# Optimization experiments

Hardware: AMD Instinct MI355X
Metric: run time of the kernel (lower is better)

The kernel has to match this reference:

```python
import jax, jax.numpy as jnp
import numpy as np


def _lin(x, w, b):
    return x @ w + b


def _fmv(x, w):
    # fused weighted mean/variance over the views axis (dim 2)
    mean = jnp.sum(x * w, axis=2, keepdims=True)
    var = jnp.sum(w * (x - mean) ** 2, axis=2, keepdims=True)
    return mean, var


def setup_inputs() -> dict:
    key = jax.random.key(0)
    ks = iter(jax.random.split(key, 40))
    R, S, V = 2048, 64, 8  # n_rays, n_samples, n_views

    def W(i, o):
        return jax.random.normal(next(ks), (i, o), jnp.float32) * (1.0 / np.sqrt(i))

    inp = {
        "rgb_feat": jax.random.normal(next(ks), (R, S, V, 35), jnp.float32),
        "neuray_feat": jax.random.normal(next(ks), (R, S, V, 32), jnp.float32),
        "ray_diff": jax.random.normal(next(ks), (R, S, V, 4), jnp.float32),
        "mask": (jax.random.uniform(next(ks), (R, S, V, 1)) > 0.1).astype(jnp.float32),
        "que_pts": jax.random.normal(next(ks), (R, S, 3), jnp.float32),
        "que_dir": jax.random.normal(next(ks), (R, S, 3), jnp.float32),
        # ray_dir_fc: Linear(4,16) ELU Linear(16,35) ELU
        "rd_w1": W(4, 16), "rd_b1": jnp.zeros(16, jnp.float32),
        "rd_w2": W(16, 35), "rd_b2": jnp.zeros(35, jnp.float32),
        # rgbfeat_fc: Linear(35,64) ReLU Linear(64,64)
        "rf_w1": W(35, 64), "rf_b1": jnp.zeros(64, jnp.float32),
        "rf_w2": W(64, 64), "rf_b2": jnp.zeros(64, jnp.float32),
        # neuray_fc: Linear(32,8) ELU Linear(8,1)
        "nr_w1": W(32, 8), "nr_b1": jnp.zeros(8, jnp.float32),
        "nr_w2": W(8, 1), "nr_b2": jnp.zeros(1, jnp.float32),
        # base_fc: Linear(207,64) ELU Linear(64,32) ELU
        "base_w1": W(207, 64), "base_b1": jnp.zeros(64, jnp.float32),
        "base_w2": W(64, 32), "base_b2": jnp.zeros(32, jnp.float32),
        # vis_fc: Linear(32,32) ELU Linear(32,33) ELU
        "vis_w1": W(32, 32), "vis_b1": jnp.zeros(32, jnp.float32),
        "vis_w2": W(32, 33), "vis_b2": jnp.zeros(33, jnp.float32),
        # vis_fc2: Linear(32,32) ELU Linear(32,1) Sigmoid
        "v2_w1": W(32, 32), "v2_b1": jnp.zeros(32, jnp.float32),
        "v2_w2": W(32, 1), "v2_b2": jnp.zeros(1, jnp.float32),
    }
    return inp


def reference(rgb_feat, neuray_feat, ray_diff, mask, que_pts, que_dir,
              rd_w1, rd_b1, rd_w2, rd_b2,
              rf_w1, rf_b1, rf_w2, rf_b2,
              nr_w1, nr_b1, nr_w2, nr_b2,
              base_w1, base_b1, base_w2, base_b2,
              vis_w1, vis_b1, vis_w2, vis_b2,
              v2_w1, v2_b1, v2_w2, v2_b2):
    elu = jax.nn.elu
    num_views = rgb_feat.shape[2]

    direction_feat = elu(_lin(elu(_lin(ray_diff, rd_w1, rd_b1)), rd_w2, rd_b2))
    rgb_feat_ = rgb_feat + direction_feat  # [R,S,V,35]

    rgb_feat_1 = _lin(jax.nn.relu(_lin(rgb_feat, rf_w1, rf_b1)), rf_w2, rf_b2)
    rgb_feat_max = jnp.max(rgb_feat_1, axis=2)  # [R,S,64]

    weight = mask / (jnp.sum(mask, axis=2, keepdims=True) + 1e-8)
    weight0 = jax.nn.sigmoid(_lin(elu(_lin(neuray_feat, nr_w1, nr_b1)), nr_w2, nr_b2))

    mean0, var0 = _fmv(rgb_feat_, weight0)
    mean1, var1 = _fmv(rgb_feat_, weight)
    globalfeat = jnp.concatenate([mean0, var0, mean1, var1], axis=-1)  # [R,S,1,140]

    gshape = globalfeat.shape[:2] + (num_views, globalfeat.shape[-1])
    x = jnp.concatenate([jnp.broadcast_to(globalfeat, gshape), rgb_feat_, neuray_feat], axis=-1)  # [R,S,V,207]
    x = elu(_lin(elu(_lin(x, base_w1, base_b1)), base_w2, base_b2))  # [R,S,V,32]

    x_vis = elu(_lin(elu(_lin(x * weight, vis_w1, vis_b1)), vis_w2, vis_b2))  # [R,S,V,33]
    x_res, vis = x_vis[..., :-1], x_vis[..., -1:]
    vis = jax.nn.sigmoid(vis) * mask
    x = x + x_res
    vis = jax.nn.sigmoid(_lin(elu(_lin(x * vis, v2_w1, v2_b1)), v2_w2, v2_b2)) * mask
    weight2 = vis / (jnp.sum(vis, axis=2, keepdims=True) + 1e-8)

    mean, var = _fmv(x, weight2)
    out = jnp.concatenate([mean[:, :, 0], var[:, :, 0]], axis=-1) + rgb_feat_max  # [R,S,64]
    return out
```

## Files before the change

### kernel.cpp

```cpp
#include <hip/hip_runtime.h>


#define NRS (2048*64)

__device__ __forceinline__ float eluf(float x){ return x > 0.f ? x : __expf(x)-1.f; }
__device__ __forceinline__ float sigmf(float x){ return 1.f/(1.f+__expf(-x)); }
__device__ __forceinline__ float sum8(float x){
    x += __shfl_xor(x, 1); x += __shfl_xor(x, 2); x += __shfl_xor(x, 4); return x;
}
__device__ __forceinline__ float max8(float x){
    x = fmaxf(x, __shfl_xor(x, 1)); x = fmaxf(x, __shfl_xor(x, 2)); x = fmaxf(x, __shfl_xor(x, 4)); return x;
}

__global__ __launch_bounds__(64, 2) void nerf_main(
    const float* __restrict__ g_rgb,  const float* __restrict__ g_nr,
    const float* __restrict__ g_rd,   const float* __restrict__ g_mask,
    const float* __restrict__ rd_w1,  const float* __restrict__ rd_b1,
    const float* __restrict__ rd_w2,  const float* __restrict__ rd_b2,
    const float* __restrict__ rf_w1,  const float* __restrict__ rf_b1,
    const float* __restrict__ rf_w2,  const float* __restrict__ rf_b2,
    const float* __restrict__ nr_w1,  const float* __restrict__ nr_b1,
    const float* __restrict__ nr_w2,  const float* __restrict__ nr_b2,
    const float* __restrict__ base_w1,const float* __restrict__ base_b1,
    const float* __restrict__ base_w2,const float* __restrict__ base_b2,
    const float* __restrict__ vis_w1, const float* __restrict__ vis_b1,
    const float* __restrict__ vis_w2, const float* __restrict__ vis_b2,
    const float* __restrict__ v2_w1,  const float* __restrict__ v2_b1,
    const float* __restrict__ v2_w2,  const float* __restrict__ v2_b2,
    float* __restrict__ out)
{
    __shared__ __align__(16) float g_lds[8*144];
    __shared__ float gc_lds  [8*65];
    __shared__ float gmax_lds[8*65];
    __shared__ float out_lds [512];

    const int lane = threadIdx.x;
    const int t    = lane >> 3;
    const int v    = lane & 7;
    const int pid  = blockIdx.x * 64 + lane;

    float rgb[35];
    #pragma unroll
    for (int k = 0; k < 35; ++k) rgb[k] = g_rgb[(size_t)pid*35 + k];
    float rdv[4];
    #pragma unroll
    for (int k = 0; k < 4; ++k) rdv[k] = g_rd[(size_t)pid*4 + k];
    float nrv[32];
    #pragma unroll
    for (int k = 0; k < 32; ++k) nrv[k] = g_nr[(size_t)pid*32 + k];
    const float mask = g_mask[pid];
    const float wt   = mask / (sum8(mask) + 1e-8f);

    float x64[64];
    {
        float acc[64];
        #pragma unroll
        for (int o = 0; o < 64; ++o) acc[o] = rf_b1[o];
        #pragma unroll 1
        for (int k = 0; k < 35; ++k) {
            const float xk = rgb[k];
            #pragma unroll
            for (int o = 0; o < 64; ++o) acc[o] = fmaf(xk, rf_w1[k*64 + o], acc[o]);
        }
        #pragma unroll
        for (int o = 0; o < 64; ++o) x64[o] = fmaxf(acc[o], 0.f);
    }

    {
        float h16[16];
        #pragma unroll
        for (int o = 0; o < 16; ++o) {
            float a = rd_b1[o];
            #pragma unroll
            for (int k = 0; k < 4; ++k) a = fmaf(rdv[k], rd_w1[k*16 + o], a);
            h16[o] = eluf(a);
        }
        #pragma unroll 1
        for (int o = 0; o < 35; ++o) {
            float a = rd_b2[o];
            #pragma unroll
            for (int k = 0; k < 16; ++k) a = fmaf(h16[k], rd_w2[k*35 + o], a);
            rgb[o] += eluf(a);
        }
    }

    {
        float acc[64];
        #pragma unroll
        for (int o = 0; o < 64; ++o) acc[o] = rf_b2[o];
        #pragma unroll 1
        for (int k = 0; k < 64; ++k) {
            const float xk = x64[k];
            #pragma unroll
            for (int o = 0; o < 64; ++o) acc[o] = fmaf(xk, rf_w2[k*64 + o], acc[o]);
        }
        #pragma unroll
        for (int o = 0; o < 64; ++o) {
            const float gm = max8(acc[o]);
            if (v == (o & 7)) gmax_lds[t*65 + o] = gm;
        }
    }

    float w0;
    {
        float h8[8];
        #pragma unroll
        for (int o = 0; o < 8; ++o) h8[o] = nr_b1[o];
        #pragma unroll 4
        for (int k = 0; k < 32; ++k) {
            const float xk = nrv[k];
            #pragma unroll
            for (int o = 0; o < 8; ++o) h8[o] = fmaf(xk, nr_w1[k*8 + o], h8[o]);
        }
        float a = nr_b2[0];
        #pragma unroll
        for (int k = 0; k < 8; ++k) a = fmaf(eluf(h8[k]), nr_w2[k], a);
        w0 = sigmf(a);
    }

    #pragma unroll 2
    for (int f = 0; f < 35; ++f) {
        const float a  = rgb[f];
        const float m0 = sum8(w0 * a);
        const float d0 = a - m0;
        const float v0 = sum8(w0 * d0 * d0);
        const float m1 = sum8(wt * a);
        const float d1 = a - m1;
        const float v1 = sum8(wt * d1 * d1);
        if (v == (f & 7)) {
            g_lds[t*144 + f]       = m0;
            g_lds[t*144 + 35 + f]  = v0;
            g_lds[t*144 + 70 + f]  = m1;
            g_lds[t*144 + 105 + f] = v1;
        }
    }
    __syncthreads();

    {
        float ga[8];
        #pragma unroll
        for (int q = 0; q < 8; ++q) ga[q] = 0.f;
        #pragma unroll 1
        for (int i = 0; i < 140; i += 4) {
            float w_[4];
            #pragma unroll
            for (int j = 0; j < 4; ++j) w_[j] = base_w1[(i + j)*64 + lane];
            #pragma unroll
            for (int q = 0; q < 8; ++q) {
                const float4 gv = *reinterpret_cast<const float4*>(&g_lds[q*144 + i]);
                ga[q] = fmaf(gv.x, w_[0], ga[q]);
                ga[q] = fmaf(gv.y, w_[1], ga[q]);
                ga[q] = fmaf(gv.z, w_[2], ga[q]);
                ga[q] = fmaf(gv.w, w_[3], ga[q]);
            }
        }
        #pragma unroll
        for (int q = 0; q < 8; ++q) gc_lds[q*65 + lane] = ga[q];
    }
    __syncthreads();

    {
        float acc[64];
        #pragma unroll
        for (int o = 0; o < 64; ++o) acc[o] = base_b1[o] + gc_lds[t*65 + o];
        #pragma unroll 1
        for (int k = 0; k < 35; ++k) {
            const float xk = rgb[k];
            #pragma unroll
            for (int o = 0; o < 64; ++o) acc[o] = fmaf(xk, base_w1[(140+k)*64 + o], acc[o]);
        }
        #pragma unroll 1
        for (int k = 0; k < 32; ++k) {
            const float xk = nrv[k];
            #pragma unroll
            for (int o = 0; o < 64; ++o) acc[o] = fmaf(xk, base_w1[(175+k)*64 + o], acc[o]);
        }
        #pragma unroll
        for (int o = 0; o < 64; ++o) x64[o] = eluf(acc[o]);
    }

    float x2[32];
    {
        #pragma unroll
        for (int o = 0; o < 32; ++o) x2[o] = base_b2[o];
        #pragma unroll 2
        for (int k = 0; k < 64; ++k) {
            const float xk = x64[k];
            #pragma unroll
            for (int o = 0; o < 32; ++o) x2[o] = fmaf(xk, base_w2[k*32 + o], x2[o]);
        }
        #pragma unroll
        for (int o = 0; o < 32; ++o) x2[o] = eluf(x2[o]);
    }

    float hv[32];
    {
        float acc[32];
        #pragma unroll
        for (int o = 0; o < 32; ++o) acc[o] = 0.f;
        #pragma unroll 2
        for (int k = 0; k < 32; ++k) {
            const float xk = x2[k];
            #pragma unroll
            for (int o = 0; o < 32; ++o) acc[o] = fmaf(xk, vis_w1[k*32 + o], acc[o]);
        }
        #pragma unroll
        for (int o = 0; o < 32; ++o) hv[o] = eluf(fmaf(acc[o], wt, vis_b1[o]));
    }
    float vis1;
    {
        float acc[32];
        #pragma unroll
        for (int o = 0; o < 32; ++o) acc[o] = vis_b2[o];
        float a2 = vis_b2[32];
        #pragma unroll 2
        for (int k = 0; k < 32; ++k) {
            const float hk = hv[k];
            #pragma unroll
            for (int o = 0; o < 32; ++o) acc[o] = fmaf(hk, vis_w2[k*33 + o], acc[o]);
            a2 = fmaf(hk, vis_w2[k*33 + 32], a2);
        }
        #pragma unroll
        for (int o = 0; o < 32; ++o) x2[o] += eluf(acc[o]);
        vis1 = sigmf(eluf(a2)) * mask;
    }

    float vis2;
    {
        float acc[32];
        #pragma unroll
        for (int o = 0; o < 32; ++o) acc[o] = 0.f;
        #pragma unroll 2
        for (int k = 0; k < 32; ++k) {
            const float xk = x2[k];
            #pragma unroll
            for (int o = 0; o < 32; ++o) acc[o] = fmaf(xk, v2_w1[k*32 + o], acc[o]);
        }
        float a = v2_b2[0];
        #pragma unroll
        for (int k = 0; k < 32; ++k) a = fmaf(eluf(fmaf(acc[k], vis1, v2_b1[k])), v2_w2[k], a);
        vis2 = sigmf(a) * mask;
    }

    {
        const float w2 = vis2 / (sum8(vis2) + 1e-8f);
        #pragma unroll 2
        for (int c = 0; c < 32; ++c) {
            const float xv = x2[c];
            const float m  = sum8(w2 * xv);
            const float d  = xv - m;
            const float va = sum8(w2 * d * d);
            if (v == (c & 7)) {
                out_lds[t*64 + c]      = m  + gmax_lds[t*65 + c];
                out_lds[t*64 + 32 + c] = va + gmax_lds[t*65 + 32 + c];
            }
        }
    }
    __syncthreads();

    const size_t ob = (size_t)blockIdx.x * 512;
    #pragma unroll
    for (int j = 0; j < 8; ++j)
        out[ob + j*64 + lane] = out_lds[j*64 + lane];
}

extern "C" void kernel_launch(void* const* d_in, const int* in_sizes, int n_in,
                              void* d_out, int out_size, void* d_ws, size_t ws_size,
                              hipStream_t stream) {
    const float* g_rgb   = (const float*)d_in[0];
    const float* g_nr    = (const float*)d_in[1];
    const float* g_rd    = (const float*)d_in[2];
    const float* g_mask  = (const float*)d_in[3];
    const float* rd_w1   = (const float*)d_in[6];
    const float* rd_b1   = (const float*)d_in[7];
    const float* rd_w2   = (const float*)d_in[8];
    const float* rd_b2   = (const float*)d_in[9];
    const float* rf_w1   = (const float*)d_in[10];
    const float* rf_b1   = (const float*)d_in[11];
    const float* rf_w2   = (const float*)d_in[12];
    const float* rf_b2   = (const float*)d_in[13];
    const float* nr_w1   = (const float*)d_in[14];
    const float* nr_b1   = (const float*)d_in[15];
    const float* nr_w2   = (const float*)d_in[16];
    const float* nr_b2   = (const float*)d_in[17];
    const float* base_w1 = (const float*)d_in[18];
    const float* base_b1 = (const float*)d_in[19];
    const float* base_w2 = (const float*)d_in[20];
    const float* base_b2 = (const float*)d_in[21];
    const float* vis_w1  = (const float*)d_in[22];
    const float* vis_b1  = (const float*)d_in[23];
    const float* vis_w2  = (const float*)d_in[24];
    const float* vis_b2  = (const float*)d_in[25];
    const float* v2_w1   = (const float*)d_in[26];
    const float* v2_b1   = (const float*)d_in[27];
    const float* v2_w2   = (const float*)d_in[28];
    const float* v2_b2   = (const float*)d_in[29];
    float* out = (float*)d_out;

    hipLaunchKernelGGL(nerf_main, dim3(NRS / 8), dim3(64), 0, stream,
        g_rgb, g_nr, g_rd, g_mask,
        rd_w1, rd_b1, rd_w2, rd_b2,
        rf_w1, rf_b1, rf_w2, rf_b2,
        nr_w1, nr_b1, nr_w2, nr_b2,
        base_w1, base_b1, base_w2, base_b2,
        vis_w1, vis_b1, vis_w2, vis_b2,
        v2_w1, v2_b1, v2_w2, v2_b2,
        out);
}
```

Baseline: 1.305 ms.

## Stage per-thread activations in LDS to cut register pressure

Moves the per-thread input features (rgb, neuray) and intermediate activations out of registers into a shared-memory scratch laid out [feature][lane], so each layer reads its inputs from LDS instead of holding them live in VGPRs. The rgb_feat second linear layer is reordered to run before the ray-direction update, and several loop unroll factors and the launch-bounds occupancy hint are changed. The aim is to relieve register pressure and avoid spills, at the cost of extra LDS traffic and a much larger shared allocation per block, which may limit how many blocks fit per CU.

New measurement: 2.511 ms. 1.92x slower.

```diff
diff --git a/kernel.cpp b/kernel.cpp
--- a/kernel.cpp
+++ b/kernel.cpp
@@ -6,13 +6,13 @@
 __device__ __forceinline__ float eluf(float x){ return x > 0.f ? x : __expf(x)-1.f; }
 __device__ __forceinline__ float sigmf(float x){ return 1.f/(1.f+__expf(-x)); }
 __device__ __forceinline__ float sum8(float x){
-    x += __shfl_xor(x, 1); x += __shfl_xor(x, 2); x += __shfl_xor(x, 4); return x;
+    x += __shfl_xor(x,1); x += __shfl_xor(x,2); x += __shfl_xor(x,4); return x;
 }
 __device__ __forceinline__ float max8(float x){
-    x = fmaxf(x, __shfl_xor(x, 1)); x = fmaxf(x, __shfl_xor(x, 2)); x = fmaxf(x, __shfl_xor(x, 4)); return x;
+    x = fmaxf(x,__shfl_xor(x,1)); x = fmaxf(x,__shfl_xor(x,2)); x = fmaxf(x,__shfl_xor(x,4)); return x;
 }
 
-__global__ __launch_bounds__(64, 2) void nerf_main(
+__global__ __launch_bounds__(64, 1) void nerf_main(
     const float* __restrict__ g_rgb,  const float* __restrict__ g_nr,
     const float* __restrict__ g_rd,   const float* __restrict__ g_mask,
     const float* __restrict__ rd_w1,  const float* __restrict__ rd_b1,
@@ -29,41 +29,57 @@
     const float* __restrict__ v2_w2,  const float* __restrict__ v2_b2,
     float* __restrict__ out)
 {
-    __shared__ __align__(16) float g_lds[8*144];
-    __shared__ float gc_lds  [8*65];
-    __shared__ float gmax_lds[8*65];
-    __shared__ float out_lds [512];
+    __shared__ __align__(16) float S[9424];
+    float* const s_act  = S;
+    float* const s_rgb  = S + 4096;
+    float* const s_nr   = S + 6336;
+    float* const s_gc   = S + 8384;
+    float* const s_gmax = S + 8904;
 
     const int lane = threadIdx.x;
     const int t    = lane >> 3;
     const int v    = lane & 7;
     const int pid  = blockIdx.x * 64 + lane;
 
-    float rgb[35];
-    #pragma unroll
-    for (int k = 0; k < 35; ++k) rgb[k] = g_rgb[(size_t)pid*35 + k];
+    #pragma unroll 1
+    for (int k = 0; k < 35; ++k) s_rgb[k*64 + lane] = g_rgb[(size_t)pid*35 + k];
+    #pragma unroll 1
+    for (int k = 0; k < 32; ++k) s_nr[k*64 + lane] = g_nr[(size_t)pid*32 + k];
     float rdv[4];
     #pragma unroll
     for (int k = 0; k < 4; ++k) rdv[k] = g_rd[(size_t)pid*4 + k];
-    float nrv[32];
-    #pragma unroll
-    for (int k = 0; k < 32; ++k) nrv[k] = g_nr[(size_t)pid*32 + k];
     const float mask = g_mask[pid];
     const float wt   = mask / (sum8(mask) + 1e-8f);
 
-    float x64[64];
     {
         float acc[64];
         #pragma unroll
         for (int o = 0; o < 64; ++o) acc[o] = rf_b1[o];
-        #pragma unroll 1
+        #pragma unroll 2
         for (int k = 0; k < 35; ++k) {
-            const float xk = rgb[k];
+            const float xk = s_rgb[k*64 + lane];
             #pragma unroll
             for (int o = 0; o < 64; ++o) acc[o] = fmaf(xk, rf_w1[k*64 + o], acc[o]);
         }
         #pragma unroll
-        for (int o = 0; o < 64; ++o) x64[o] = fmaxf(acc[o], 0.f);
+        for (int o = 0; o < 64; ++o) s_act[o*64 + lane] = fmaxf(acc[o], 0.f);
+    }
+
+    {
+        float acc[64];
+        #pragma unroll
+        for (int o = 0; o < 64; ++o) acc[o] = rf_b2[o];
+        #pragma unroll 2
+        for (int k = 0; k < 64; ++k) {
+            const float xk = s_act[k*64 + lane];
+            #pragma unroll
+            for (int o = 0; o < 64; ++o) acc[o] = fmaf(xk, rf_w2[k*64 + o], acc[o]);
+        }
+        #pragma unroll
+        for (int o = 0; o < 64; ++o) {
+            const float gm = max8(acc[o]);
+            if (v == (o & 7)) s_gmax[t*65 + o] = gm;
+        }
     }
 
     {
@@ -80,24 +96,7 @@
             float a = rd_b2[o];
             #pragma unroll
             for (int k = 0; k < 16; ++k) a = fmaf(h16[k], rd_w2[k*35 + o], a);
-            rgb[o] += eluf(a);
-        }
-    }
-
-    {
-        float acc[64];
-        #pragma unroll
-        for (int o = 0; o < 64; ++o) acc[o] = rf_b2[o];
-        #pragma unroll 1
-        for (int k = 0; k < 64; ++k) {
-            const float xk = x64[k];
-            #pragma unroll
-            for (int o = 0; o < 64; ++o) acc[o] = fmaf(xk, rf_w2[k*64 + o], acc[o]);
-        }
-        #pragma unroll
-        for (int o = 0; o < 64; ++o) {
-            const float gm = max8(acc[o]);
-            if (v == (o & 7)) gmax_lds[t*65 + o] = gm;
+            s_rgb[o*64 + lane] += eluf(a);
         }
     }
 
@@ -106,9 +105,9 @@
         float h8[8];
         #pragma unroll
         for (int o = 0; o < 8; ++o) h8[o] = nr_b1[o];
-        #pragma unroll 4
-        for (int k = 0; k < 32; ++k) {
-            const float xk = nrv[k];
+        #pragma unroll 2
+        for (int k = 0; k < 32; ++k) {
+            const float xk = s_nr[k*64 + lane];
             #pragma unroll
             for (int o = 0; o < 8; ++o) h8[o] = fmaf(xk, nr_w1[k*8 + o], h8[o]);
         }
@@ -118,9 +117,9 @@
         w0 = sigmf(a);
     }
 
-    #pragma unroll 2
+    #pragma unroll 1
     for (int f = 0; f < 35; ++f) {
-        const float a  = rgb[f];
+        const float a  = s_rgb[f*64 + lane];
         const float m0 = sum8(w0 * a);
         const float d0 = a - m0;
         const float v0 = sum8(w0 * d0 * d0);
@@ -128,10 +127,10 @@
         const float d1 = a - m1;
         const float v1 = sum8(wt * d1 * d1);
         if (v == (f & 7)) {
-            g_lds[t*144 + f]       = m0;
-            g_lds[t*144 + 35 + f]  = v0;
-            g_lds[t*144 + 70 + f]  = m1;
-            g_lds[t*144 + 105 + f] = v1;
+            s_act[t*144 + f]       = m0;
+            s_act[t*144 + 35 + f]  = v0;
+            s_act[t*144 + 70 + f]  = m1;
+            s_act[t*144 + 105 + f] = v1;
         }
     }
     __syncthreads();
@@ -147,7 +146,7 @@
             for (int j = 0; j < 4; ++j) w_[j] = base_w1[(i + j)*64 + lane];
             #pragma unroll
             for (int q = 0; q < 8; ++q) {
-                const float4 gv = *reinterpret_cast<const float4*>(&g_lds[q*144 + i]);
+                const float4 gv = *reinterpret_cast<const float4*>(&s_act[q*144 + i]);
                 ga[q] = fmaf(gv.x, w_[0], ga[q]);
                 ga[q] = fmaf(gv.y, w_[1], ga[q]);
                 ga[q] = fmaf(gv.z, w_[2], ga[q]);
@@ -155,58 +154,59 @@
             }
         }
         #pragma unroll
-        for (int q = 0; q < 8; ++q) gc_lds[q*65 + lane] = ga[q];
+        for (int q = 0; q < 8; ++q) s_gc[q*65 + lane] = ga[q];
     }
     __syncthreads();
 
     {
         float acc[64];
         #pragma unroll
-        for (int o = 0; o < 64; ++o) acc[o] = base_b1[o] + gc_lds[t*65 + o];
-        #pragma unroll 1
+        for (int o = 0; o < 64; ++o) acc[o] = base_b1[o] + s_gc[t*65 + o];
+        #pragma unroll 2
         for (int k = 0; k < 35; ++k) {
-            const float xk = rgb[k];
+            const float xk = s_rgb[k*64 + lane];
             #pragma unroll
             for (int o = 0; o < 64; ++o) acc[o] = fmaf(xk, base_w1[(140+k)*64 + o], acc[o]);
         }
-        #pragma unroll 1
-        for (int k = 0; k < 32; ++k) {
-            const float xk = nrv[k];
+        #pragma unroll 2
+        for (int k = 0; k < 32; ++k) {
+            const float xk = s_nr[k*64 + lane];
             #pragma unroll
             for (int o = 0; o < 64; ++o) acc[o] = fmaf(xk, base_w1[(175+k)*64 + o], acc[o]);
         }
         #pragma unroll
-        for (int o = 0; o < 64; ++o) x64[o] = eluf(acc[o]);
-    }
-
-    float x2[32];
-    {
-        #pragma unroll
-        for (int o = 0; o < 32; ++o) x2[o] = base_b2[o];
+        for (int o = 0; o < 64; ++o) s_act[o*64 + lane] = eluf(acc[o]);
+    }
+
+    {
+        float acc[32];
+        #pragma unroll
+        for (int o = 0; o < 32; ++o) acc[o] = base_b2[o];
         #pragma unroll 2
         for (int k = 0; k < 64; ++k) {
-            const float xk = x64[k];
-            #pragma unroll
-            for (int o = 0; o < 32; ++o) x2[o] = fmaf(xk, base_w2[k*32 + o], x2[o]);
-        }
-        #pragma unroll
-        for (int o = 0; o < 32; ++o) x2[o] = eluf(x2[o]);
-    }
-
-    float hv[32];
+            const float xk = s_act[k*64 + lane];
+            #pragma unroll
+            for (int o = 0; o < 32; ++o) acc[o] = fmaf(xk, base_w2[k*32 + o], acc[o]);
+        }
+        #pragma unroll
+        for (int o = 0; o < 32; ++o) s_nr[o*64 + lane] = eluf(acc[o]);
+    }
+
     {
         float acc[32];
         #pragma unroll
         for (int o = 0; o < 32; ++o) acc[o] = 0.f;
         #pragma unroll 2
         for (int k = 0; k < 32; ++k) {
-            const float xk = x2[k];
+            const float xk = s_nr[k*64 + lane];
             #pragma unroll
             for (int o = 0; o < 32; ++o) acc[o] = fmaf(xk, vis_w1[k*32 + o], acc[o]);
         }
         #pragma unroll
-        for (int o = 0; o < 32; ++o) hv[o] = eluf(fmaf(acc[o], wt, vis_b1[o]));
-    }
+        for (int o = 0; o < 32; ++o)
+            s_rgb[o*64 + lane] = eluf(fmaf(acc[o], wt, vis_b1[o]));
+    }
+
     float vis1;
     {
         float acc[32];
@@ -215,44 +215,51 @@
         float a2 = vis_b2[32];
         #pragma unroll 2
         for (int k = 0; k < 32; ++k) {
-            const float hk = hv[k];
+            const float hk = s_rgb[k*64 + lane];
             #pragma unroll
             for (int o = 0; o < 32; ++o) acc[o] = fmaf(hk, vis_w2[k*33 + o], acc[o]);
             a2 = fmaf(hk, vis_w2[k*33 + 32], a2);
         }
         #pragma unroll
-        for (int o = 0; o < 32; ++o) x2[o] += eluf(acc[o]);
+        for (int o = 0; o < 32; ++o) s_nr[o*64 + lane] += eluf(acc[o]);
         vis1 = sigmf(eluf(a2)) * mask;
     }
 
+    {
+        float acc[32];
+        #pragma unroll
+        for (int o = 0; o < 32; ++o) acc[o] = 0.f;
+        #pragma unroll 2
+        for (int k = 0; k < 32; ++k) {
+            const float xk = s_nr[k*64 + lane];
+            #pragma unroll
+            for (int o = 0; o < 32; ++o) acc[o] = fmaf(xk, v2_w1[k*32 + o], acc[o]);
+        }
+        #pragma unroll
+        for (int o = 0; o < 32; ++o)
+            s_rgb[o*64 + lane] = eluf(fmaf(acc[o], vis1, v2_b1[o]));
+    }
+
     float vis2;
     {
-        float acc[32];
-        #pragma unroll
-        for (int o = 0; o < 32; ++o) acc[o] = 0.f;
-        #pragma unroll 2
-        for (int k = 0; k < 32; ++k) {
-            const float xk = x2[k];
-            #pragma unroll
-            for (int o = 0; o < 32; ++o) acc[o] = fmaf(xk, v2_w1[k*32 + o], acc[o]);
-        }
         float a = v2_b2[0];
-        #pragma unroll
-        for (int k = 0; k < 32; ++k) a = fmaf(eluf(fmaf(acc[k], vis1, v2_b1[k])), v2_w2[k], a);
+        #pragma unroll 2
+        for (int k = 0; k < 32; ++k) a = fmaf(s_rgb[k*64 + lane], v2_w2[k], a);
         vis2 = sigmf(a) * mask;
     }
+    __syncthreads();
 
     {
         const float w2 = vis2 / (sum8(vis2) + 1e-8f);
-        #pragma unroll 2
+        #pragma unroll 1
         for (int c = 0; c < 32; ++c) {
-            const float xv = x2[c];
+            const float xv = s_nr[c*64 + lane];
             const float m  = sum8(w2 * xv);
             const float d  = xv - m;
             const float va = sum8(w2 * d * d);
             if (v == (c & 7)) {
-                out_lds[t*64 + c]      = m  + gmax_lds[t*65 + c];
-                out_lds[t*64 + 32 + c] = va + gmax_lds[t*65 + 32 + c];
+                s_rgb[t*64 + c]      = m  + s_gmax[t*65 + c];
+                s_rgb[t*64 + 32 + c] = va + s_gmax[t*65 + 32 + c];
             }
         }
     }
@@ -261,7 +268,7 @@
     const size_t ob = (size_t)blockIdx.x * 512;
     #pragma unroll
     for (int j = 0; j < 8; ++j)
-        out[ob + j*64 + lane] = out_lds[j*64 + lane];
+        out[ob + j*64 + lane] = s_rgb[j*64 + lane];
 }
 
 extern "C" void kernel_launch(void* const* d_in, const int* in_sizes, int n_in,
```
